# Kernel tuning notes

Measured on AMD Instinct MI355X. Metric: run time of the kernel, lower is better.

## Reference

```python
import jax, jax.numpy as jnp
import numpy as np

N_NODES = 50000
N_USERS = 10000
N_STATE = 1024
N_T1 = 2048
N_T2 = 2048
N_EDGES = 4096


def setup_inputs() -> dict:
    key = jax.random.key(0)
    ks = jax.random.split(key, 10)
    d = N_STATE
    s_u = jax.random.normal(ks[0], (N_USERS, d), jnp.float32)
    x = jax.random.normal(ks[1], (N_NODES, d), jnp.float32)
    # Deterministic graph on which the original torch code is well-defined:
    # POI node 0 has one outgoing edge (edge 0) to tail node 1.
    # Tail node 1 receives edges from heads [0, 2, 3, ..., N_EDGES] in edge order,
    # so list-order in the torch loop aligns with edge-index order.
    heads = np.concatenate([[0], np.arange(2, N_EDGES + 1)]).astype(np.int64)
    tails = np.ones(N_EDGES, dtype=np.int64)
    edge_index = jnp.asarray(np.stack([heads, tails]))
    edge_attr = jax.random.normal(ks[2], (N_EDGES, d), jnp.float32)
    T = jax.random.normal(ks[3], (N_T1, N_T2), jnp.float32)
    u = lambda k, s: jax.random.uniform(k, s, jnp.float32, -1.0, 1.0)
    W_u = u(ks[4], (d, 1))
    W_p = u(ks[5], (d, 1))
    W_T_1 = u(ks[6], (d, N_T1))
    W_T_2 = u(ks[7], (N_T2, 1))
    b_T = u(ks[8], (d, 1))
    W_p_ = u(ks[9], (1, d))
    return dict(s_u=s_u, x=x, edge_attr=edge_attr, T=T, W_u=W_u, W_p=W_p,
                W_T_1=W_T_1, W_T_2=W_T_2, b_T=b_T, W_p_=W_p_,
                edge_index=edge_index, user_index=7, POI_index=0)


def reference(s_u, x, edge_attr, T, W_u, W_p, W_T_1, W_T_2, b_T, W_p_,
              edge_index, user_index, POI_index):
    N, d = x.shape
    heads, tails = edge_index[0], edge_index[1]
    # temporal context vector: sigmoid(W_T_1 @ T @ W_T_2 + b_T), shape (d,)
    t_vec = jax.nn.sigmoid(W_T_1 @ T @ W_T_2 + b_T)[:, 0]
    cur_user = s_u[user_index]   # (d,)
    cur_POI = x[POI_index]       # (d,)
    # user update: u' = sigmoid(u + W_u * (h_P . T'))
    s_u = s_u.at[user_index].set(
        jax.nn.sigmoid(cur_user + W_u[:, 0] * jnp.dot(cur_POI, t_vec)))
    # visited POI update: h' = sigmoid(h + W_p * (u . T'))
    new_POI = jax.nn.sigmoid(cur_POI + W_p[:, 0] * jnp.dot(cur_user, t_vec))
    x = x.at[POI_index].set(new_POI)
    # tail entities of the visited POI: x[tail] = new_POI + edge_attr[e]
    rel_mask = heads == POI_index
    dummy = jnp.zeros((1, d), x.dtype)
    tgt = jnp.where(rel_mask, tails, N)  # route masked-out edges to dummy row
    x = jnp.concatenate([x, dummy], 0).at[tgt].set(new_POI[None, :] + edge_attr)[:N]
    # neighboring POIs: edges whose tail is in the tail set; replicate the original
    # neigh_rel[POI_index] = False / neigh_index.remove(POI_index) pair, which by
    # construction both drop the edge at position POI_index.
    is_tail = jnp.zeros((N + 1,), bool).at[tgt].set(True)[:N]
    neigh_mask = is_tail[tails].at[POI_index].set(False)  # (E,)
    h_emb = x[heads]                        # (E, d), tail-updated embeddings
    scal = (h_emb - edge_attr) @ W_p_[0]    # (E,)  W_p_ . (x[head] - r)
    vals = jax.nn.sigmoid(h_emb + scal[:, None])
    tgt2 = jnp.where(neigh_mask, heads, N)
    x = jnp.concatenate([x, dummy], 0).at[tgt2].set(vals)[:N]
    return (s_u, x)
```

## Files before the change

kernel.cpp:

```cpp
#include <hip/hip_runtime.h>
#include <math.h>

#define D 1024

__device__ __forceinline__ float sigmoidf_(float v) {
    return 1.0f / (1.0f + expf(-v));
}

__device__ __forceinline__ float block_reduce_sum256(float v) {
    #pragma unroll
    for (int off = 32; off; off >>= 1) v += __shfl_down(v, off, 64);
    __shared__ float sm[4];
    int lane = threadIdx.x & 63, w = threadIdx.x >> 6;
    if (lane == 0) sm[w] = v;
    __syncthreads();
    return sm[0] + sm[1] + sm[2] + sm[3];
}

__global__ void k_matvec_T(const float* __restrict__ T,
                           const float* __restrict__ w,
                           float* __restrict__ tmp) {
    int row = blockIdx.x;
    const float4* Tr = (const float4*)(T + (size_t)row * 2048);
    const float4* wv = (const float4*)w;
    float acc = 0.f;
    for (int i = threadIdx.x; i < 512; i += 256) {
        float4 a = Tr[i], b = wv[i];
        acc += a.x * b.x + a.y * b.y + a.z * b.z + a.w * b.w;
    }
    float s = block_reduce_sum256(acc);
    if (threadIdx.x == 0) tmp[row] = s;
}

__global__ void k_tvec(const float* __restrict__ W_T_1,
                       const float* __restrict__ tmp,
                       const float* __restrict__ b_T,
                       float* __restrict__ t_vec) {
    int row = blockIdx.x;
    const float4* Wr = (const float4*)(W_T_1 + (size_t)row * 2048);
    const float4* tv = (const float4*)tmp;
    float acc = 0.f;
    for (int i = threadIdx.x; i < 512; i += 256) {
        float4 a = Wr[i], b = tv[i];
        acc += a.x * b.x + a.y * b.y + a.z * b.z + a.w * b.w;
    }
    float s = block_reduce_sum256(acc);
    if (threadIdx.x == 0) t_vec[row] = sigmoidf_(s + b_T[row]);
}

__global__ void k_dots(const float* __restrict__ x,
                       const float* __restrict__ s_u,
                       const float* __restrict__ t_vec,
                       const int* __restrict__ user_ptr,
                       const int* __restrict__ POI_ptr,
                       float* __restrict__ dots) {
    const float* src = (blockIdx.x == 0)
        ? x + (size_t)POI_ptr[0] * D
        : s_u + (size_t)user_ptr[0] * D;
    const float4* a = (const float4*)src;
    const float4* b = (const float4*)t_vec;
    float acc = 0.f;
    float4 p = a[threadIdx.x], q = b[threadIdx.x];
    acc = p.x * q.x + p.y * q.y + p.z * q.z + p.w * q.w;
    float s = block_reduce_sum256(acc);
    if (threadIdx.x == 0) dots[blockIdx.x] = s;
}

__global__ void k_newrows(const float* __restrict__ s_u,
                          const float* __restrict__ x,
                          const float* __restrict__ W_u,
                          const float* __restrict__ W_p,
                          const int* __restrict__ user_ptr,
                          const int* __restrict__ POI_ptr,
                          const float* __restrict__ dots,
                          float* __restrict__ new_user,
                          float* __restrict__ new_POI) {
    int i = blockIdx.x * 256 + threadIdx.x;
    int user = user_ptr[0], POI = POI_ptr[0];
    float dotP = dots[0], dotU = dots[1];
    new_user[i] = sigmoidf_(s_u[(size_t)user * D + i] + W_u[i] * dotP);
    new_POI[i]  = sigmoidf_(x[(size_t)POI * D + i] + W_p[i] * dotU);
}

__global__ void k_copy4(const float4* __restrict__ src,
                        float4* __restrict__ dst, int n4) {
    int i = blockIdx.x * blockDim.x + threadIdx.x;
    int stride = gridDim.x * blockDim.x;
    for (; i < n4; i += stride) dst[i] = src[i];
}

__global__ void k_fix(float* __restrict__ out_su, float* __restrict__ out_x,
                      const float* __restrict__ new_user,
                      const float* __restrict__ new_POI,
                      const int* __restrict__ user_ptr,
                      const int* __restrict__ POI_ptr) {
    int i = blockIdx.x * 256 + threadIdx.x;
    out_su[(size_t)user_ptr[0] * D + i] = new_user[i];
    out_x[(size_t)POI_ptr[0] * D + i] = new_POI[i];
}

__global__ void k_tail(const int* __restrict__ edge_index,
                       const float* __restrict__ edge_attr,
                       const float* __restrict__ new_POI,
                       const int* __restrict__ POI_ptr,
                       float* __restrict__ out_x,
                       int* __restrict__ is_tail, int E) {
    int e = blockIdx.x;
    if (edge_index[e] != POI_ptr[0]) return;
    int t = edge_index[E + e];
    if (threadIdx.x == 0) is_tail[t] = 1;
    float4* dst = (float4*)(out_x + (size_t)t * D);
    const float4* ea = (const float4*)(edge_attr + (size_t)e * D);
    const float4* np = (const float4*)new_POI;
    float4 a = np[threadIdx.x], b = ea[threadIdx.x];
    dst[threadIdx.x] = make_float4(a.x + b.x, a.y + b.y, a.z + b.z, a.w + b.w);
}

__global__ void k_neigh(const int* __restrict__ edge_index,
                        const float* __restrict__ edge_attr,
                        const float* __restrict__ Wp_row,
                        const int* __restrict__ is_tail,
                        const int* __restrict__ POI_ptr,
                        float* __restrict__ out_x, int E) {
    int e = blockIdx.x;
    if (e == POI_ptr[0]) return;
    int t = edge_index[E + e];
    if (!is_tail[t]) return;
    int h = edge_index[e];
    float4* xr = (float4*)(out_x + (size_t)h * D);
    const float4* ea = (const float4*)(edge_attr + (size_t)e * D);
    const float4* wv = (const float4*)Wp_row;
    float4 xv = xr[threadIdx.x];
    float4 ev = ea[threadIdx.x];
    float4 w = wv[threadIdx.x];
    float acc = (xv.x - ev.x) * w.x + (xv.y - ev.y) * w.y +
                (xv.z - ev.z) * w.z + (xv.w - ev.w) * w.w;
    float scal = block_reduce_sum256(acc);
    float4 o;
    o.x = sigmoidf_(xv.x + scal);
    o.y = sigmoidf_(xv.y + scal);
    o.z = sigmoidf_(xv.z + scal);
    o.w = sigmoidf_(xv.w + scal);
    xr[threadIdx.x] = o;
}

extern "C" void kernel_launch(void* const* d_in, const int* in_sizes, int n_in,
                              void* d_out, int out_size, void* d_ws, size_t ws_size,
                              hipStream_t stream) {
    const float* s_u       = (const float*)d_in[0];
    const float* x         = (const float*)d_in[1];
    const float* edge_attr = (const float*)d_in[2];
    const float* T         = (const float*)d_in[3];
    const float* W_u       = (const float*)d_in[4];
    const float* W_p       = (const float*)d_in[5];
    const float* W_T_1     = (const float*)d_in[6];
    const float* W_T_2     = (const float*)d_in[7];
    const float* b_T       = (const float*)d_in[8];
    const float* W_p_      = (const float*)d_in[9];
    const int*   edge_index = (const int*)d_in[10];
    const int*   user_ptr   = (const int*)d_in[11];
    const int*   POI_ptr    = (const int*)d_in[12];

    const int E       = in_sizes[10] / 2;
    const int N_users = in_sizes[0] / D;
    const int N       = in_sizes[1] / D;

    float* out_su = (float*)d_out;
    float* out_x  = out_su + (size_t)N_users * D;

    float* ws_f     = (float*)d_ws;
    float* tmp      = ws_f;
    float* t_vec    = ws_f + 2048;
    float* dots     = ws_f + 3072;
    float* new_user = ws_f + 3584;
    float* new_POI  = ws_f + 4608;
    int*   is_tail  = (int*)(ws_f + 5632);

    hipMemsetAsync(is_tail, 0, sizeof(int) * (size_t)N, stream);

    k_matvec_T<<<2048, 256, 0, stream>>>(T, W_T_2, tmp);
    k_tvec<<<1024, 256, 0, stream>>>(W_T_1, tmp, b_T, t_vec);
    k_dots<<<2, 256, 0, stream>>>(x, s_u, t_vec, user_ptr, POI_ptr, dots);
    k_newrows<<<4, 256, 0, stream>>>(s_u, x, W_u, W_p, user_ptr, POI_ptr, dots,
                                     new_user, new_POI);

    k_copy4<<<4096, 256, 0, stream>>>((const float4*)s_u, (float4*)out_su,
                                      (int)((size_t)N_users * D / 4));
    k_copy4<<<4096, 256, 0, stream>>>((const float4*)x, (float4*)out_x,
                                      (int)((size_t)N * D / 4));
    k_fix<<<4, 256, 0, stream>>>(out_su, out_x, new_user, new_POI,
                                 user_ptr, POI_ptr);
    k_tail<<<E, 256, 0, stream>>>(edge_index, edge_attr, new_POI, POI_ptr,
                                  out_x, is_tail, E);
    k_neigh<<<E, 256, 0, stream>>>(edge_index, edge_attr, W_p_, is_tail,
                                   POI_ptr, out_x, E);
}
```

Before: 131.8 us.

## Fuse setup, copies and scatter fixups into fewer kernels with edge ownership maps

Replaces the dots, newrows, fix, tail and neigh kernels and the is_tail memset with a single-block setup kernel. That kernel builds per-node tail_edge and neigh_edge ownership maps with atomics and computes the new user and POI rows. The two output copies become one kernel, and a single fixup kernel handles the user/POI row writes, the tail writes and the neighbor updates by recomputing the head embedding instead of reading the intermediate output. This removes several launches and the memset, and cuts the dependency between the tail and neigh passes. The cost is a serial single-block setup over E edges, and the last-writer semantics must now be resolved through atomicMax.

```diff
diff --git a/kernel.cpp b/kernel.cpp
--- a/kernel.cpp
+++ b/kernel.cpp
@@ -1,5 +1,6 @@
 #include <hip/hip_runtime.h>
 #include <math.h>
+#include <limits.h>
 
 #define D 1024
 
@@ -14,7 +15,23 @@
     int lane = threadIdx.x & 63, w = threadIdx.x >> 6;
     if (lane == 0) sm[w] = v;
     __syncthreads();
-    return sm[0] + sm[1] + sm[2] + sm[3];
+    float s = sm[0] + sm[1] + sm[2] + sm[3];
+    __syncthreads();
+    return s;
+}
+
+__device__ __forceinline__ float block_reduce_sum1024(float v) {
+    #pragma unroll
+    for (int off = 32; off; off >>= 1) v += __shfl_down(v, off, 64);
+    __shared__ float sm[16];
+    int lane = threadIdx.x & 63, w = threadIdx.x >> 6;
+    if (lane == 0) sm[w] = v;
+    __syncthreads();
+    float s = 0.f;
+    #pragma unroll
+    for (int i = 0; i < 16; i++) s += sm[i];
+    __syncthreads();
+    return s;
 }
 
 __global__ void k_matvec_T(const float* __restrict__ T,
@@ -48,100 +65,120 @@
     if (threadIdx.x == 0) t_vec[row] = sigmoidf_(s + b_T[row]);
 }
 
-__global__ void k_dots(const float* __restrict__ x,
-                       const float* __restrict__ s_u,
-                       const float* __restrict__ t_vec,
-                       const int* __restrict__ user_ptr,
-                       const int* __restrict__ POI_ptr,
-                       float* __restrict__ dots) {
-    const float* src = (blockIdx.x == 0)
-        ? x + (size_t)POI_ptr[0] * D
-        : s_u + (size_t)user_ptr[0] * D;
-    const float4* a = (const float4*)src;
-    const float4* b = (const float4*)t_vec;
-    float acc = 0.f;
-    float4 p = a[threadIdx.x], q = b[threadIdx.x];
-    acc = p.x * q.x + p.y * q.y + p.z * q.z + p.w * q.w;
-    float s = block_reduce_sum256(acc);
-    if (threadIdx.x == 0) dots[blockIdx.x] = s;
-}
-
-__global__ void k_newrows(const float* __restrict__ s_u,
-                          const float* __restrict__ x,
-                          const float* __restrict__ W_u,
-                          const float* __restrict__ W_p,
-                          const int* __restrict__ user_ptr,
-                          const int* __restrict__ POI_ptr,
-                          const float* __restrict__ dots,
-                          float* __restrict__ new_user,
-                          float* __restrict__ new_POI) {
-    int i = blockIdx.x * 256 + threadIdx.x;
-    int user = user_ptr[0], POI = POI_ptr[0];
-    float dotP = dots[0], dotU = dots[1];
-    new_user[i] = sigmoidf_(s_u[(size_t)user * D + i] + W_u[i] * dotP);
-    new_POI[i]  = sigmoidf_(x[(size_t)POI * D + i] + W_p[i] * dotU);
-}
-
-__global__ void k_copy4(const float4* __restrict__ src,
-                        float4* __restrict__ dst, int n4) {
+__global__ void k_setup(const int* __restrict__ edge_index,
+                        const float* __restrict__ x,
+                        const float* __restrict__ s_u,
+                        const float* __restrict__ t_vec,
+                        const float* __restrict__ W_u,
+                        const float* __restrict__ W_p,
+                        const int* __restrict__ user_ptr,
+                        const int* __restrict__ POI_ptr,
+                        int* __restrict__ tail_edge,
+                        int* __restrict__ neigh_edge,
+                        float* __restrict__ new_user,
+                        float* __restrict__ new_POI, int E) {
+    const int tid = threadIdx.x;
+    const int POI = POI_ptr[0], user = user_ptr[0];
+
+    for (int e = tid; e < E; e += 1024) {
+        int h = edge_index[e], t = edge_index[E + e];
+        tail_edge[h] = -1;  tail_edge[t] = -1;
+        neigh_edge[h] = -1; neigh_edge[t] = -1;
+    }
+    if (tid == 0) { tail_edge[POI] = -1; neigh_edge[POI] = -1; }
+    __syncthreads();
+
+    for (int e = tid; e < E; e += 1024)
+        if (edge_index[e] == POI) atomicMax(&tail_edge[edge_index[E + e]], e);
+    __syncthreads();
+
+    for (int e = tid; e < E; e += 1024) {
+        if (e == POI) continue;
+        int t = edge_index[E + e];
+        int te = atomicMax(&tail_edge[t], INT_MIN);
+        if (te >= 0) atomicMax(&neigh_edge[edge_index[e]], e);
+    }
+    __syncthreads();
+
+    float xv = x[(size_t)POI * D + tid];
+    float uv = s_u[(size_t)user * D + tid];
+    float tv = t_vec[tid];
+    float dotP = block_reduce_sum1024(xv * tv);
+    float dotU = block_reduce_sum1024(uv * tv);
+    new_user[tid] = sigmoidf_(uv + W_u[tid] * dotP);
+    new_POI[tid]  = sigmoidf_(xv + W_p[tid] * dotU);
+}
+
+__global__ void k_copy_all(const float4* __restrict__ su,
+                           const float4* __restrict__ xx,
+                           float4* __restrict__ out,
+                           int n4_su, int n4_total) {
     int i = blockIdx.x * blockDim.x + threadIdx.x;
     int stride = gridDim.x * blockDim.x;
-    for (; i < n4; i += stride) dst[i] = src[i];
-}
-
-__global__ void k_fix(float* __restrict__ out_su, float* __restrict__ out_x,
-                      const float* __restrict__ new_user,
-                      const float* __restrict__ new_POI,
-                      const int* __restrict__ user_ptr,
-                      const int* __restrict__ POI_ptr) {
-    int i = blockIdx.x * 256 + threadIdx.x;
-    out_su[(size_t)user_ptr[0] * D + i] = new_user[i];
-    out_x[(size_t)POI_ptr[0] * D + i] = new_POI[i];
-}
-
-__global__ void k_tail(const int* __restrict__ edge_index,
-                       const float* __restrict__ edge_attr,
-                       const float* __restrict__ new_POI,
-                       const int* __restrict__ POI_ptr,
-                       float* __restrict__ out_x,
-                       int* __restrict__ is_tail, int E) {
-    int e = blockIdx.x;
-    if (edge_index[e] != POI_ptr[0]) return;
-    int t = edge_index[E + e];
-    if (threadIdx.x == 0) is_tail[t] = 1;
-    float4* dst = (float4*)(out_x + (size_t)t * D);
-    const float4* ea = (const float4*)(edge_attr + (size_t)e * D);
-    const float4* np = (const float4*)new_POI;
-    float4 a = np[threadIdx.x], b = ea[threadIdx.x];
-    dst[threadIdx.x] = make_float4(a.x + b.x, a.y + b.y, a.z + b.z, a.w + b.w);
-}
-
-__global__ void k_neigh(const int* __restrict__ edge_index,
+    for (; i < n4_total; i += stride)
+        out[i] = (i < n4_su) ? su[i] : xx[i - n4_su];
+}
+
+__global__ void k_fixup(const int* __restrict__ edge_index,
                         const float* __restrict__ edge_attr,
+                        const float* __restrict__ x,
                         const float* __restrict__ Wp_row,
-                        const int* __restrict__ is_tail,
+                        const float* __restrict__ new_user,
+                        const float* __restrict__ new_POI,
+                        const int* __restrict__ tail_edge,
+                        const int* __restrict__ neigh_edge,
+                        const int* __restrict__ user_ptr,
                         const int* __restrict__ POI_ptr,
+                        float* __restrict__ out_su,
                         float* __restrict__ out_x, int E) {
-    int e = blockIdx.x;
-    if (e == POI_ptr[0]) return;
-    int t = edge_index[E + e];
-    if (!is_tail[t]) return;
-    int h = edge_index[e];
-    float4* xr = (float4*)(out_x + (size_t)h * D);
-    const float4* ea = (const float4*)(edge_attr + (size_t)e * D);
-    const float4* wv = (const float4*)Wp_row;
-    float4 xv = xr[threadIdx.x];
-    float4 ev = ea[threadIdx.x];
-    float4 w = wv[threadIdx.x];
-    float acc = (xv.x - ev.x) * w.x + (xv.y - ev.y) * w.y +
-                (xv.z - ev.z) * w.z + (xv.w - ev.w) * w.w;
-    float scal = block_reduce_sum256(acc);
-    float4 o;
-    o.x = sigmoidf_(xv.x + scal);
-    o.y = sigmoidf_(xv.y + scal);
-    o.z = sigmoidf_(xv.z + scal);
-    o.w = sigmoidf_(xv.w + scal);
-    xr[threadIdx.x] = o;
+    const int e = blockIdx.x;
+    const int tid = threadIdx.x;
+    const int POI = POI_ptr[0];
+    const float4* np_ = (const float4*)new_POI;
+
+    if (e == E) {
+        int user = user_ptr[0];
+        ((float4*)(out_su + (size_t)user * D))[tid] =
+            ((const float4*)new_user)[tid];
+        if (tail_edge[POI] < 0 && neigh_edge[POI] < 0)
+            ((float4*)(out_x + (size_t)POI * D))[tid] = np_[tid];
+        return;
+    }
+
+    const int h = edge_index[e], t = edge_index[E + e];
+
+    if (h == POI && tail_edge[t] == e && neigh_edge[t] < 0) {
+        const float4* ea = (const float4*)(edge_attr + (size_t)e * D);
+        float4 a = np_[tid], b = ea[tid];
+        ((float4*)(out_x + (size_t)t * D))[tid] =
+            make_float4(a.x + b.x, a.y + b.y, a.z + b.z, a.w + b.w);
+    }
+
+    if (e != POI && tail_edge[t] >= 0 && neigh_edge[h] == e) {
+        float4 hv;
+        int be = tail_edge[h];
+        if (be >= 0) {
+            const float4* eb = (const float4*)(edge_attr + (size_t)be * D);
+            float4 a = np_[tid], b = eb[tid];
+            hv = make_float4(a.x + b.x, a.y + b.y, a.z + b.z, a.w + b.w);
+        } else if (h == POI) {
+            hv = np_[tid];
+        } else {
+            hv = ((const float4*)(x + (size_t)h * D))[tid];
+        }
+        const float4* ea = (const float4*)(edge_attr + (size_t)e * D);
+        float4 ev = ea[tid];
+        float4 w = ((const float4*)Wp_row)[tid];
+        float acc = (hv.x - ev.x) * w.x + (hv.y - ev.y) * w.y +
+                    (hv.z - ev.z) * w.z + (hv.w - ev.w) * w.w;
+        float scal = block_reduce_sum256(acc);
+        float4 o;
+        o.x = sigmoidf_(hv.x + scal);
+        o.y = sigmoidf_(hv.y + scal);
+        o.z = sigmoidf_(hv.z + scal);
+        o.w = sigmoidf_(hv.w + scal);
+        ((float4*)(out_x + (size_t)h * D))[tid] = o;
+    }
 }
 
 extern "C" void kernel_launch(void* const* d_in, const int* in_sizes, int n_in,
@@ -168,30 +205,26 @@
     float* out_su = (float*)d_out;
     float* out_x  = out_su + (size_t)N_users * D;
 
-    float* ws_f     = (float*)d_ws;
-    float* tmp      = ws_f;
-    float* t_vec    = ws_f + 2048;
-    float* dots     = ws_f + 3072;
-    float* new_user = ws_f + 3584;
-    float* new_POI  = ws_f + 4608;
-    int*   is_tail  = (int*)(ws_f + 5632);
-
-    hipMemsetAsync(is_tail, 0, sizeof(int) * (size_t)N, stream);
+    float* ws_f      = (float*)d_ws;
+    float* tmp       = ws_f;
+    float* t_vec     = ws_f + 2048;
+    float* new_user  = ws_f + 3072;
+    float* new_POI   = ws_f + 4096;
+    int*   tail_edge = (int*)(ws_f + 5120);
+    int*   neigh_edge = tail_edge + N;
 
     k_matvec_T<<<2048, 256, 0, stream>>>(T, W_T_2, tmp);
     k_tvec<<<1024, 256, 0, stream>>>(W_T_1, tmp, b_T, t_vec);
-    k_dots<<<2, 256, 0, stream>>>(x, s_u, t_vec, user_ptr, POI_ptr, dots);
-    k_newrows<<<4, 256, 0, stream>>>(s_u, x, W_u, W_p, user_ptr, POI_ptr, dots,
-                                     new_user, new_POI);
-
-    k_copy4<<<4096, 256, 0, stream>>>((const float4*)s_u, (float4*)out_su,
-                                      (int)((size_t)N_users * D / 4));
-    k_copy4<<<4096, 256, 0, stream>>>((const float4*)x, (float4*)out_x,
-                                      (int)((size_t)N * D / 4));
-    k_fix<<<4, 256, 0, stream>>>(out_su, out_x, new_user, new_POI,
-                                 user_ptr, POI_ptr);
-    k_tail<<<E, 256, 0, stream>>>(edge_index, edge_attr, new_POI, POI_ptr,
-                                  out_x, is_tail, E);
-    k_neigh<<<E, 256, 0, stream>>>(edge_index, edge_attr, W_p_, is_tail,
-                                   POI_ptr, out_x, E);
-}
+    k_setup<<<1, 1024, 0, stream>>>(edge_index, x, s_u, t_vec, W_u, W_p,
+                                    user_ptr, POI_ptr, tail_edge, neigh_edge,
+                                    new_user, new_POI, E);
+
+    const int n4_su = (int)((size_t)N_users * D / 4);
+    const int n4_total = n4_su + (int)((size_t)N * D / 4);
+    k_copy_all<<<4096, 256, 0, stream>>>((const float4*)s_u, (const float4*)x,
+                                         (float4*)d_out, n4_su, n4_total);
+
+    k_fixup<<<E + 1, 256, 0, stream>>>(edge_index, edge_attr, x, W_p_,
+                                       new_user, new_POI, tail_edge, neigh_edge,
+                                       user_ptr, POI_ptr, out_su, out_x, E);
+}
```

New measurement: 125.5 us. 4.8% less time.
